# Kernel tuning notes

Measured on AMD Instinct MI355X. Metric: run time of the kernel, lower is better.

## Reference

```python
import jax, jax.numpy as jnp
import numpy as np

B, L, H, NH = 128, 512, 128, 2
HD = H // NH
NEG = -2.0**32 + 1  # matches torch paddings value


def _split_heads(x):
    # [B, L, H] -> [NH, B, L, HD]; equivalent to torch.cat(torch.split(x, HD, dim=2), dim=0)
    return x.reshape(B, L, NH, HD).transpose(2, 0, 1, 3)


def setup_inputs() -> dict:
    key = jax.random.key(0)
    ks = jax.random.split(key, 9)
    f = lambda k, s: jax.random.normal(k, s, dtype=jnp.float32)
    return {
        "queries": f(ks[0], (B, L, H)),
        "keys": f(ks[1], (B, L, H)),
        "neighbor_matrix": f(ks[2], (B, L, H)),
        "neighAt_matrix": f(ks[3], (B, L, H)),
        "abs_pos_K": f(ks[4], (B, L, H)),
        "abs_pos_V": f(ks[5], (B, L, H)),
        "Q_w": f(ks[6], (H, H)) * 0.05, "Q_b": jnp.zeros((H,), jnp.float32),
        "K_w": f(ks[7], (H, H)) * 0.05, "K_b": jnp.zeros((H,), jnp.float32),
        "V_w": f(ks[8], (H, H)) * 0.05, "V_b": jnp.zeros((H,), jnp.float32),
        # causal mask: True = masked, as used in NISRec (~tril)
        "attn_mask": ~jnp.tril(jnp.ones((L, L), dtype=bool)),
    }


def reference(queries, keys, neighbor_matrix, neighAt_matrix, abs_pos_K, abs_pos_V,
              Q_w, Q_b, K_w, K_b, V_w, V_b, attn_mask):
    Q = _split_heads(queries @ Q_w.T + Q_b)          # [NH,B,L,HD]
    K = _split_heads(keys @ K_w.T + K_b)
    V = _split_heads(keys @ V_w.T + V_b)
    nbr = _split_heads(neighbor_matrix)
    nat = _split_heads(neighAt_matrix)
    pk = _split_heads(abs_pos_K)
    pv = _split_heads(abs_pos_V)
    # sum of four Q.matmul(X^T) terms == Q.matmul((K+nbr+nat+pk)^T); same math, one GEMM
    logits = jnp.einsum('hbqd,hbkd->hbqk', Q, K + nbr + nat + pk)
    logits = logits / jnp.sqrt(jnp.asarray(HD, logits.dtype))
    logits = jnp.where(attn_mask[None, None, :, :], jnp.asarray(NEG, logits.dtype), logits)
    w = jax.nn.softmax(logits, axis=-1)  # dropout off (eval)
    # sum of four attn.matmul(X) terms == attn.matmul(V+nbr+nat+pv)
    out = jnp.einsum('hbqk,hbkd->hbqd', w, V + nbr + nat + pv)
    # merge heads back: torch.cat(torch.split(outputs, B, dim=0), dim=2)
    return out.transpose(1, 2, 0, 3).reshape(B, L, H)
```

## Files before the change

kernel.cpp:

```cpp
#include <hip/hip_runtime.h>

typedef __attribute__((ext_vector_type(8))) short bf16x8;
typedef __attribute__((ext_vector_type(4))) short bf16x4;
typedef __attribute__((ext_vector_type(4))) float f32x4;

#define NB 128
#define LL 512
#define HH 128
#define HDIM 64
#define NROWS (NB * LL)

__device__ __forceinline__ unsigned short f2b(float f) {
  unsigned int x = __float_as_uint(f);
  x = (x + 0x7fffu + ((x >> 16) & 1u)) >> 16;
  return (unsigned short)x;
}

__device__ __forceinline__ bf16x8 load8_cvt(const float* p) {
  float4 a = *(const float4*)p;
  float4 b = *(const float4*)(p + 4);
  bf16x8 r;
  r[0] = (short)f2b(a.x); r[1] = (short)f2b(a.y);
  r[2] = (short)f2b(a.z); r[3] = (short)f2b(a.w);
  r[4] = (short)f2b(b.x); r[5] = (short)f2b(b.y);
  r[6] = (short)f2b(b.z); r[7] = (short)f2b(b.w);
  return r;
}

#if __has_builtin(__builtin_amdgcn_mfma_f32_16x16x16bf16_1k)
__device__ __forceinline__ f32x4 mfma16(bf16x4 a, bf16x4 b, f32x4 c) {
  return __builtin_amdgcn_mfma_f32_16x16x16bf16_1k(a, b, c, 0, 0, 0);
}
#else
__device__ __forceinline__ f32x4 mfma16(bf16x4 a, bf16x4 b, f32x4 c) {
  asm volatile("s_nop 1\n\t"
               "v_mfma_f32_16x16x16_bf16 %0, %1, %2, %0\n\t"
               "s_nop 7\n\t"
               "s_nop 7"
               : "+v"(c) : "v"(a), "v"(b));
  return c;
}
#endif

__device__ __forceinline__ f32x4 mfma32(bf16x8 a, bf16x8 b, f32x4 c) {
  return __builtin_amdgcn_mfma_f32_16x16x32_bf16(a, b, c, 0, 0, 0);
}

__global__ __launch_bounds__(256) void wcvt_kernel(
    const float* __restrict__ Qw, const float* __restrict__ Kw,
    const float* __restrict__ Vw, unsigned short* __restrict__ Wb) {
  const int i = blockIdx.x * 256 + threadIdx.x;
  const float* src = (i < 4096) ? Qw : (i < 8192) ? Kw : Vw;
  const int off = (i & 4095) << 2;
  float4 v = *(const float4*)(src + off);
  ushort4 u;
  u.x = f2b(v.x); u.y = f2b(v.y); u.z = f2b(v.z); u.w = f2b(v.w);
  *(ushort4*)(Wb + ((size_t)i << 2)) = u;
}

__global__ __launch_bounds__(512) void fused_kernel(
    const float* __restrict__ queries, const float* __restrict__ keys,
    const float* __restrict__ nbr, const float* __restrict__ nat,
    const float* __restrict__ pk, const float* __restrict__ pv,
    const unsigned short* __restrict__ Wb, const float* __restrict__ Qbias,
    const float* __restrict__ Vbias, unsigned short* __restrict__ Vt,
    float* __restrict__ out) {
  __shared__ unsigned short wlds[2 * 128 * 128];
  __shared__ unsigned short klds[512 * 64];

  const int id = blockIdx.x;
  const int h = id >> 7;
  const int b = id & 127;
  const int tid = threadIdx.x;
  const int lane = tid & 63;
  const int w = tid >> 6;
  const int g = lane >> 4;
  const int qi = lane & 15;
  const int rswz = (qi & 7) << 4;

#pragma unroll
  for (int i = 0; i < 8; ++i) {
    const int byte = (tid + i * 512) * 16;
    const int row = (byte >> 8) & 127;
    *(bf16x8*)((char*)wlds + (byte ^ ((row & 7) << 4))) =
        *(const bf16x8*)((const char*)Wb + 32768 + byte);
  }
  __syncthreads();

  for (int rg = 0; rg < 4; ++rg) {
    const int l = w * 64 + rg * 16 + qi;
    const long roff = ((long)b * LL + l) * 128;

    bf16x8 xk[4];
#pragma unroll
    for (int kt = 0; kt < 4; ++kt)
      xk[kt] = load8_cvt(keys + roff + kt * 32 + g * 8);

    f32x4 accK[4];
#pragma unroll
    for (int ct = 0; ct < 4; ++ct) {
      accK[ct] = f32x4{0.f, 0.f, 0.f, 0.f};
      const int rw = h * 64 + ct * 16 + qi;
#pragma unroll
      for (int kt = 0; kt < 4; ++kt) {
        const int byte = rw * 256 + ((kt * 64 + g * 16) ^ rswz);
        bf16x8 wf = *(const bf16x8*)((const char*)wlds + byte);
        accK[ct] = mfma32(wf, xk[kt], accK[ct]);
      }
    }

    float4 tmp[4];
#pragma unroll
    for (int ct = 0; ct < 4; ++ct) {
      const int dl = ct * 16 + 4 * g;
      const int cg = h * 64 + dl;
      const float4 nb4 = *(const float4*)(nbr + roff + cg);
      const float4 na4 = *(const float4*)(nat + roff + cg);
      const float4 pk4 = *(const float4*)(pk + roff + cg);
      float4 t;
      t.x = nb4.x + na4.x; t.y = nb4.y + na4.y;
      t.z = nb4.z + na4.z; t.w = nb4.w + na4.w;
      tmp[ct] = t;
      ushort4 u;
      u.x = f2b(accK[ct][0] + t.x + pk4.x);
      u.y = f2b(accK[ct][1] + t.y + pk4.y);
      u.z = f2b(accK[ct][2] + t.z + pk4.z);
      u.w = f2b(accK[ct][3] + t.w + pk4.w);
      const int kb = l * 128 + dl * 2;
      *(ushort4*)((char*)klds + (kb ^ ((l & 7) << 4))) = u;
    }

    f32x4 accV[4];
#pragma unroll
    for (int ct = 0; ct < 4; ++ct) {
      accV[ct] = f32x4{0.f, 0.f, 0.f, 0.f};
      const int rw = h * 64 + ct * 16 + qi;
#pragma unroll
      for (int kt = 0; kt < 4; ++kt) {
        const int byte = 32768 + rw * 256 + ((kt * 64 + g * 16) ^ rswz);
        bf16x8 wf = *(const bf16x8*)((const char*)wlds + byte);
        accV[ct] = mfma32(wf, xk[kt], accV[ct]);
      }
    }
#pragma unroll
    for (int ct = 0; ct < 4; ++ct) {
      const int dl = ct * 16 + 4 * g;
      const int cg = h * 64 + dl;
      const float4 pv4 = *(const float4*)(pv + roff + cg);
      unsigned short* vp = Vt + (((long)h * NB + b) * HDIM + dl) * LL + l;
      vp[0 * LL] = f2b(accV[ct][0] + tmp[ct].x + pv4.x);
      vp[1 * LL] = f2b(accV[ct][1] + tmp[ct].y + pv4.y);
      vp[2 * LL] = f2b(accV[ct][2] + tmp[ct].z + pv4.z);
      vp[3 * LL] = f2b(accV[ct][3] + tmp[ct].w + pv4.w);
    }
  }

  __syncthreads();

#pragma unroll
  for (int i = 0; i < 4; ++i) {
    const int byte = (tid + i * 512) * 16;
    const int row = (byte >> 8) & 127;
    *(bf16x8*)((char*)wlds + (byte ^ ((row & 7) << 4))) =
        *(const bf16x8*)((const char*)Wb + byte);
  }
  __syncthreads();

  float vbe[4];
#pragma unroll
  for (int dt = 0; dt < 4; ++dt) vbe[dt] = Vbias[h * 64 + dt * 16 + qi];

  char* slot = (char*)wlds + 32768 + w * 2048;
  const unsigned short* Vbase = Vt + ((long)h * NB + b) * HDIM * LL;

  for (int half = 0; half < 2; ++half) {
    const int c = half ? w : 15 - w;
    const int qbase = c * 32;
    const int ntile = (c >> 1) + 1;

    bf16x8 qf[2][2];
#pragma unroll
    for (int q2 = 0; q2 < 2; ++q2) {
      const int l = qbase + q2 * 16 + qi;
      const long roff = ((long)b * LL + l) * 128;
      bf16x8 xq[4];
#pragma unroll
      for (int kt = 0; kt < 4; ++kt)
        xq[kt] = load8_cvt(queries + roff + kt * 32 + g * 8);
      f32x4 aq[4];
#pragma unroll
      for (int ct = 0; ct < 4; ++ct) {
        aq[ct] = f32x4{0.f, 0.f, 0.f, 0.f};
        const int rw = h * 64 + ct * 16 + qi;
#pragma unroll
        for (int kt = 0; kt < 4; ++kt) {
          const int byte = rw * 256 + ((kt * 64 + g * 16) ^ rswz);
          bf16x8 wf = *(const bf16x8*)((const char*)wlds + byte);
          aq[ct] = mfma32(wf, xq[kt], aq[ct]);
        }
      }
#pragma unroll
      for (int ct = 0; ct < 4; ++ct) {
        const int dl = ct * 16 + 4 * g;
        const float4 bv = *(const float4*)(Qbias + h * 64 + dl);
        ushort4 u;
        u.x = f2b(aq[ct][0] + bv.x);
        u.y = f2b(aq[ct][1] + bv.y);
        u.z = f2b(aq[ct][2] + bv.z);
        u.w = f2b(aq[ct][3] + bv.w);
        const int bb = qi * 128 + dl * 2;
        *(ushort4*)(slot + (bb ^ ((qi & 7) << 4))) = u;
      }
      asm volatile("s_waitcnt lgkmcnt(0)" ::: "memory");
      __builtin_amdgcn_sched_barrier(0);
      qf[q2][0] = *(const bf16x8*)(slot + ((qi * 128 + g * 16) ^ ((qi & 7) << 4)));
      qf[q2][1] = *(const bf16x8*)(slot + ((qi * 128 + 64 + g * 16) ^ ((qi & 7) << 4)));
    }

    f32x4 o[2][4];
#pragma unroll
    for (int q2 = 0; q2 < 2; ++q2)
#pragma unroll
      for (int dt = 0; dt < 4; ++dt) o[q2][dt] = f32x4{0.f, 0.f, 0.f, 0.f};
    float m[2] = {-1e30f, -1e30f};
    float lsum[2] = {0.f, 0.f};

    for (int it = 0; it < ntile; ++it) {
      const int k0 = it * 64;

      bf16x8 kf[4][2];
#pragma unroll
      for (int t = 0; t < 4; ++t) {
        const int l = k0 + t * 16 + qi;
        const int base = l * 128;
        const int sz = (l & 7) << 4;
        kf[t][0] = *(const bf16x8*)((char*)klds + ((base + g * 16) ^ sz));
        kf[t][1] = *(const bf16x8*)((char*)klds + ((base + 64 + g * 16) ^ sz));
      }

      bf16x4 vf[4][4];
#pragma unroll
      for (int dt = 0; dt < 4; ++dt)
#pragma unroll
        for (int t = 0; t < 4; ++t)
          vf[dt][t] = *(const bf16x4*)(Vbase + (dt * 16 + qi) * LL + k0 +
                                       t * 16 + 4 * g);

      f32x4 s[2][4];
#pragma unroll
      for (int q2 = 0; q2 < 2; ++q2)
#pragma unroll
        for (int t = 0; t < 4; ++t) {
          f32x4 acc = f32x4{0.f, 0.f, 0.f, 0.f};
          acc = mfma32(kf[t][0], qf[q2][0], acc);
          acc = mfma32(kf[t][1], qf[q2][1], acc);
          s[q2][t] = acc;
        }

      float alpha[2];
      bf16x4 pf[2][4];
#pragma unroll
      for (int q2 = 0; q2 < 2; ++q2) {
        const int myq = qbase + q2 * 16 + qi;
        float p[16];
        float pm = -1e30f;
#pragma unroll
        for (int t = 0; t < 4; ++t)
#pragma unroll
          for (int r = 0; r < 4; ++r) {
            float sv = s[q2][t][r] * 0.125f;
            const int key = k0 + t * 16 + 4 * g + r;
            sv = (key > myq) ? -1e30f : sv;
            p[t * 4 + r] = sv;
            pm = fmaxf(pm, sv);
          }
        pm = fmaxf(pm, __shfl_xor(pm, 16));
        pm = fmaxf(pm, __shfl_xor(pm, 32));
        const float mnew = fmaxf(m[q2], pm);
        alpha[q2] = exp2f((m[q2] - mnew) * 1.44269504f);
        float ps = 0.f;
#pragma unroll
        for (int i = 0; i < 16; ++i) {
          p[i] = exp2f((p[i] - mnew) * 1.44269504f);
          ps += p[i];
        }
        ps += __shfl_xor(ps, 16);
        ps += __shfl_xor(ps, 32);
        lsum[q2] = lsum[q2] * alpha[q2] + ps;
        m[q2] = mnew;
#pragma unroll
        for (int t = 0; t < 4; ++t) {
          pf[q2][t][0] = (short)f2b(p[t * 4 + 0]);
          pf[q2][t][1] = (short)f2b(p[t * 4 + 1]);
          pf[q2][t][2] = (short)f2b(p[t * 4 + 2]);
          pf[q2][t][3] = (short)f2b(p[t * 4 + 3]);
        }
      }

      float ar[2][4];
#pragma unroll
      for (int q2 = 0; q2 < 2; ++q2)
#pragma unroll
        for (int r = 0; r < 4; ++r) ar[q2][r] = __shfl(alpha[q2], 4 * g + r);

#pragma unroll
      for (int dt = 0; dt < 4; ++dt) {
#pragma unroll
        for (int q2 = 0; q2 < 2; ++q2) {
          o[q2][dt][0] *= ar[q2][0];
          o[q2][dt][1] *= ar[q2][1];
          o[q2][dt][2] *= ar[q2][2];
          o[q2][dt][3] *= ar[q2][3];
        }
#pragma unroll
        for (int t = 0; t < 4; ++t) {
          o[0][dt] = mfma16(pf[0][t], vf[dt][t], o[0][dt]);
          o[1][dt] = mfma16(pf[1][t], vf[dt][t], o[1][dt]);
        }
      }
    }

#pragma unroll
    for (int q2 = 0; q2 < 2; ++q2) {
      float linv[4];
#pragma unroll
      for (int r = 0; r < 4; ++r) linv[r] = 1.0f / __shfl(lsum[q2], 4 * g + r);
#pragma unroll
      for (int dt = 0; dt < 4; ++dt)
#pragma unroll
        for (int r = 0; r < 4; ++r) {
          const long row = (long)b * LL + qbase + q2 * 16 + 4 * g + r;
          out[row * HH + h * 64 + dt * 16 + qi] =
              o[q2][dt][r] * linv[r] + vbe[dt];
        }
    }
  }
}

extern "C" void kernel_launch(void* const* d_in, const int* in_sizes, int n_in,
                              void* d_out, int out_size, void* d_ws, size_t ws_size,
                              hipStream_t stream) {
  const float* queries = (const float*)d_in[0];
  const float* keys    = (const float*)d_in[1];
  const float* nbr     = (const float*)d_in[2];
  const float* nat     = (const float*)d_in[3];
  const float* pk      = (const float*)d_in[4];
  const float* pv      = (const float*)d_in[5];
  const float* Qw      = (const float*)d_in[6];
  const float* Qbias   = (const float*)d_in[7];
  const float* Kw      = (const float*)d_in[8];
  const float* Vw      = (const float*)d_in[10];
  const float* Vbias   = (const float*)d_in[11];

  unsigned short* Vt = (unsigned short*)d_ws;
  unsigned short* Wb = Vt + (size_t)2 * NB * HDIM * LL;

  wcvt_kernel<<<48, 256, 0, stream>>>(Qw, Kw, Vw, Wb);

  fused_kernel<<<256, 512, 0, stream>>>(queries, keys, nbr, nat, pk, pv, Wb,
                                        Qbias, Vbias, Vt, (float*)d_out);
}
```

Baseline: 85.76 us.

## Double block to 1024 threads with one 16-row query tile per wave

The fused kernel now runs 16 waves per block instead of 8. In the K/V projection phase each wave handles 32 rows instead of 64. In the attention phase each wave processes one 16-row query tile per half rather than two, with causal load balancing done by pairing tile j with 31-j. With only 256 blocks on the device, the goal is more resident waves per CU to hide memory and MFMA latency, and fewer live accumulators per thread. In exchange, K and V fragments are reused across fewer query rows, so each loaded fragment feeds half as many MFMAs. The 1024-thread launch bound also caps VGPRs per thread, which risks register spills.

```diff
diff --git a/kernel.cpp b/kernel.cpp
--- a/kernel.cpp
+++ b/kernel.cpp
@@ -58,7 +58,7 @@
   *(ushort4*)(Wb + ((size_t)i << 2)) = u;
 }
 
-__global__ __launch_bounds__(512) void fused_kernel(
+__global__ __launch_bounds__(1024) void fused_kernel(
     const float* __restrict__ queries, const float* __restrict__ keys,
     const float* __restrict__ nbr, const float* __restrict__ nat,
     const float* __restrict__ pk, const float* __restrict__ pv,
@@ -79,16 +79,17 @@
   const int rswz = (qi & 7) << 4;
 
 #pragma unroll
-  for (int i = 0; i < 8; ++i) {
-    const int byte = (tid + i * 512) * 16;
+  for (int i = 0; i < 4; ++i) {
+    const int byte = (tid + i * 1024) * 16;
     const int row = (byte >> 8) & 127;
     *(bf16x8*)((char*)wlds + (byte ^ ((row & 7) << 4))) =
         *(const bf16x8*)((const char*)Wb + 32768 + byte);
   }
   __syncthreads();
 
-  for (int rg = 0; rg < 4; ++rg) {
-    const int l = w * 64 + rg * 16 + qi;
+#pragma unroll
+  for (int rg = 0; rg < 2; ++rg) {
+    const int l = w * 32 + rg * 16 + qi;
     const long roff = ((long)b * LL + l) * 128;
 
     bf16x8 xk[4];
@@ -158,8 +159,8 @@
   __syncthreads();
 
 #pragma unroll
-  for (int i = 0; i < 4; ++i) {
-    const int byte = (tid + i * 512) * 16;
+  for (int i = 0; i < 2; ++i) {
+    const int byte = (tid + i * 1024) * 16;
     const int row = (byte >> 8) & 127;
     *(bf16x8*)((char*)wlds + (byte ^ ((row & 7) << 4))) =
         *(const bf16x8*)((const char*)Wb + byte);
@@ -174,56 +175,51 @@
   const unsigned short* Vbase = Vt + ((long)h * NB + b) * HDIM * LL;
 
   for (int half = 0; half < 2; ++half) {
-    const int c = half ? w : 15 - w;
-    const int qbase = c * 32;
-    const int ntile = (c >> 1) + 1;
-
-    bf16x8 qf[2][2];
-#pragma unroll
-    for (int q2 = 0; q2 < 2; ++q2) {
-      const int l = qbase + q2 * 16 + qi;
-      const long roff = ((long)b * LL + l) * 128;
-      bf16x8 xq[4];
-#pragma unroll
-      for (int kt = 0; kt < 4; ++kt)
-        xq[kt] = load8_cvt(queries + roff + kt * 32 + g * 8);
-      f32x4 aq[4];
-#pragma unroll
-      for (int ct = 0; ct < 4; ++ct) {
-        aq[ct] = f32x4{0.f, 0.f, 0.f, 0.f};
-        const int rw = h * 64 + ct * 16 + qi;
-#pragma unroll
-        for (int kt = 0; kt < 4; ++kt) {
-          const int byte = rw * 256 + ((kt * 64 + g * 16) ^ rswz);
-          bf16x8 wf = *(const bf16x8*)((const char*)wlds + byte);
-          aq[ct] = mfma32(wf, xq[kt], aq[ct]);
-        }
-      }
-#pragma unroll
-      for (int ct = 0; ct < 4; ++ct) {
-        const int dl = ct * 16 + 4 * g;
-        const float4 bv = *(const float4*)(Qbias + h * 64 + dl);
-        ushort4 u;
-        u.x = f2b(aq[ct][0] + bv.x);
-        u.y = f2b(aq[ct][1] + bv.y);
-        u.z = f2b(aq[ct][2] + bv.z);
-        u.w = f2b(aq[ct][3] + bv.w);
-        const int bb = qi * 128 + dl * 2;
-        *(ushort4*)(slot + (bb ^ ((qi & 7) << 4))) = u;
-      }
-      asm volatile("s_waitcnt lgkmcnt(0)" ::: "memory");
-      __builtin_amdgcn_sched_barrier(0);
-      qf[q2][0] = *(const bf16x8*)(slot + ((qi * 128 + g * 16) ^ ((qi & 7) << 4)));
-      qf[q2][1] = *(const bf16x8*)(slot + ((qi * 128 + 64 + g * 16) ^ ((qi & 7) << 4)));
-    }
-
-    f32x4 o[2][4];
-#pragma unroll
-    for (int q2 = 0; q2 < 2; ++q2)
-#pragma unroll
-      for (int dt = 0; dt < 4; ++dt) o[q2][dt] = f32x4{0.f, 0.f, 0.f, 0.f};
-    float m[2] = {-1e30f, -1e30f};
-    float lsum[2] = {0.f, 0.f};
+    const int j = half ? w : 31 - w;
+    const int qbase = j * 16;
+    const int myq = qbase + qi;
+    const int ntile = (j >> 2) + 1;
+
+    const long roff = ((long)b * LL + qbase + qi) * 128;
+    bf16x8 xq[4];
+#pragma unroll
+    for (int kt = 0; kt < 4; ++kt)
+      xq[kt] = load8_cvt(queries + roff + kt * 32 + g * 8);
+    f32x4 aq[4];
+#pragma unroll
+    for (int ct = 0; ct < 4; ++ct) {
+      aq[ct] = f32x4{0.f, 0.f, 0.f, 0.f};
+      const int rw = h * 64 + ct * 16 + qi;
+#pragma unroll
+      for (int kt = 0; kt < 4; ++kt) {
+        const int byte = rw * 256 + ((kt * 64 + g * 16) ^ rswz);
+        bf16x8 wf = *(const bf16x8*)((const char*)wlds + byte);
+        aq[ct] = mfma32(wf, xq[kt], aq[ct]);
+      }
+    }
+#pragma unroll
+    for (int ct = 0; ct < 4; ++ct) {
+      const int dl = ct * 16 + 4 * g;
+      const float4 bv = *(const float4*)(Qbias + h * 64 + dl);
+      ushort4 u;
+      u.x = f2b(aq[ct][0] + bv.x);
+      u.y = f2b(aq[ct][1] + bv.y);
+      u.z = f2b(aq[ct][2] + bv.z);
+      u.w = f2b(aq[ct][3] + bv.w);
+      const int bb = qi * 128 + dl * 2;
+      *(ushort4*)(slot + (bb ^ ((qi & 7) << 4))) = u;
+    }
+    asm volatile("s_waitcnt lgkmcnt(0)" ::: "memory");
+    __builtin_amdgcn_sched_barrier(0);
+    const bf16x8 qf0 =
+        *(const bf16x8*)(slot + ((qi * 128 + g * 16) ^ ((qi & 7) << 4)));
+    const bf16x8 qf1 =
+        *(const bf16x8*)(slot + ((qi * 128 + 64 + g * 16) ^ ((qi & 7) << 4)));
+
+    f32x4 o[4];
+#pragma unroll
+    for (int dt = 0; dt < 4; ++dt) o[dt] = f32x4{0.f, 0.f, 0.f, 0.f};
+    float m = -1e30f, lsum = 0.f;
 
     for (int it = 0; it < ntile; ++it) {
       const int k0 = it * 64;
@@ -246,94 +242,77 @@
           vf[dt][t] = *(const bf16x4*)(Vbase + (dt * 16 + qi) * LL + k0 +
                                        t * 16 + 4 * g);
 
-      f32x4 s[2][4];
-#pragma unroll
-      for (int q2 = 0; q2 < 2; ++q2)
-#pragma unroll
-        for (int t = 0; t < 4; ++t) {
-          f32x4 acc = f32x4{0.f, 0.f, 0.f, 0.f};
-          acc = mfma32(kf[t][0], qf[q2][0], acc);
-          acc = mfma32(kf[t][1], qf[q2][1], acc);
-          s[q2][t] = acc;
+      f32x4 s[4];
+#pragma unroll
+      for (int t = 0; t < 4; ++t) {
+        f32x4 acc = f32x4{0.f, 0.f, 0.f, 0.f};
+        acc = mfma32(kf[t][0], qf0, acc);
+        acc = mfma32(kf[t][1], qf1, acc);
+        s[t] = acc;
+      }
+
+      float p[16];
+      float pm = -1e30f;
+#pragma unroll
+      for (int t = 0; t < 4; ++t)
+#pragma unroll
+        for (int r = 0; r < 4; ++r) {
+          float sv = s[t][r] * 0.125f;
+          const int key = k0 + t * 16 + 4 * g + r;
+          sv = (key > myq) ? -1e30f : sv;
+          p[t * 4 + r] = sv;
+          pm = fmaxf(pm, sv);
         }
-
-      float alpha[2];
-      bf16x4 pf[2][4];
-#pragma unroll
-      for (int q2 = 0; q2 < 2; ++q2) {
-        const int myq = qbase + q2 * 16 + qi;
-        float p[16];
-        float pm = -1e30f;
+      pm = fmaxf(pm, __shfl_xor(pm, 16));
+      pm = fmaxf(pm, __shfl_xor(pm, 32));
+      const float mnew = fmaxf(m, pm);
+      const float alpha = exp2f((m - mnew) * 1.44269504f);
+      float ps = 0.f;
+#pragma unroll
+      for (int i = 0; i < 16; ++i) {
+        p[i] = exp2f((p[i] - mnew) * 1.44269504f);
+        ps += p[i];
+      }
+      ps += __shfl_xor(ps, 16);
+      ps += __shfl_xor(ps, 32);
+      lsum = lsum * alpha + ps;
+      m = mnew;
+
+      bf16x4 pf[4];
+#pragma unroll
+      for (int t = 0; t < 4; ++t) {
+        pf[t][0] = (short)f2b(p[t * 4 + 0]);
+        pf[t][1] = (short)f2b(p[t * 4 + 1]);
+        pf[t][2] = (short)f2b(p[t * 4 + 2]);
+        pf[t][3] = (short)f2b(p[t * 4 + 3]);
+      }
+
+      float ar[4];
+#pragma unroll
+      for (int r = 0; r < 4; ++r) ar[r] = __shfl(alpha, 4 * g + r);
+
+#pragma unroll
+      for (int dt = 0; dt < 4; ++dt) {
+        o[dt][0] *= ar[0];
+        o[dt][1] *= ar[1];
+        o[dt][2] *= ar[2];
+        o[dt][3] *= ar[3];
 #pragma unroll
         for (int t = 0; t < 4; ++t)
-#pragma unroll
-          for (int r = 0; r < 4; ++r) {
-            float sv = s[q2][t][r] * 0.125f;
-            const int key = k0 + t * 16 + 4 * g + r;
-            sv = (key > myq) ? -1e30f : sv;
-            p[t * 4 + r] = sv;
-            pm = fmaxf(pm, sv);
-          }
-        pm = fmaxf(pm, __shfl_xor(pm, 16));
-        pm = fmaxf(pm, __shfl_xor(pm, 32));
-        const float mnew = fmaxf(m[q2], pm);
-        alpha[q2] = exp2f((m[q2] - mnew) * 1.44269504f);
-        float ps = 0.f;
-#pragma unroll
-        for (int i = 0; i < 16; ++i) {
-          p[i] = exp2f((p[i] - mnew) * 1.44269504f);
-          ps += p[i];
-        }
-        ps += __shfl_xor(ps, 16);
-        ps += __shfl_xor(ps, 32);
-        lsum[q2] = lsum[q2] * alpha[q2] + ps;
-        m[q2] = mnew;
-#pragma unroll
-        for (int t = 0; t < 4; ++t) {
-          pf[q2][t][0] = (short)f2b(p[t * 4 + 0]);
-          pf[q2][t][1] = (short)f2b(p[t * 4 + 1]);
-          pf[q2][t][2] = (short)f2b(p[t * 4 + 2]);
-          pf[q2][t][3] = (short)f2b(p[t * 4 + 3]);
-        }
-      }
-
-      float ar[2][4];
-#pragma unroll
-      for (int q2 = 0; q2 < 2; ++q2)
-#pragma unroll
-        for (int r = 0; r < 4; ++r) ar[q2][r] = __shfl(alpha[q2], 4 * g + r);
-
-#pragma unroll
-      for (int dt = 0; dt < 4; ++dt) {
-#pragma unroll
-        for (int q2 = 0; q2 < 2; ++q2) {
-          o[q2][dt][0] *= ar[q2][0];
-          o[q2][dt][1] *= ar[q2][1];
-          o[q2][dt][2] *= ar[q2][2];
-          o[q2][dt][3] *= ar[q2][3];
-        }
-#pragma unroll
-        for (int t = 0; t < 4; ++t) {
-          o[0][dt] = mfma16(pf[0][t], vf[dt][t], o[0][dt]);
-          o[1][dt] = mfma16(pf[1][t], vf[dt][t], o[1][dt]);
-        }
-      }
-    }
-
-#pragma unroll
-    for (int q2 = 0; q2 < 2; ++q2) {
-      float linv[4];
-#pragma unroll
-      for (int r = 0; r < 4; ++r) linv[r] = 1.0f / __shfl(lsum[q2], 4 * g + r);
-#pragma unroll
-      for (int dt = 0; dt < 4; ++dt)
-#pragma unroll
-        for (int r = 0; r < 4; ++r) {
-          const long row = (long)b * LL + qbase + q2 * 16 + 4 * g + r;
-          out[row * HH + h * 64 + dt * 16 + qi] =
-              o[q2][dt][r] * linv[r] + vbe[dt];
-        }
-    }
+          o[dt] = mfma16(pf[t], vf[dt][t], o[dt]);
+      }
+    }
+
+    float linv[4];
+#pragma unroll
+    for (int r = 0; r < 4; ++r) linv[r] = 1.0f / __shfl(lsum, 4 * g + r);
+#pragma unroll
+    for (int dt = 0; dt < 4; ++dt)
+#pragma unroll
+      for (int r = 0; r < 4; ++r) {
+        const long row = (long)b * LL + qbase + 4 * g + r;
+        out[row * HH + h * 64 + dt * 16 + qi] = o[dt][r] * linv[r] + vbe[dt];
+      }
   }
 }
 
@@ -357,6 +336,6 @@
 
   wcvt_kernel<<<48, 256, 0, stream>>>(Qw, Kw, Vw, Wb);
 
-  fused_kernel<<<256, 512, 0, stream>>>(queries, keys, nbr, nat, pk, pv, Wb,
-                                        Qbias, Vbias, Vt, (float*)d_out);
-}
+  fused_kernel<<<256, 1024, 0, stream>>>(queries, keys, nbr, nat, pk, pv, Wb,
+                                         Qbias, Vbias, Vt, (float*)d_out);
+}
```

Result: slower. 132.3 us (+54.3%).

## Software-pipeline key and stream global loads across row groups with manual waitcnt

Applied to the files above, without the earlier changes.

Replaces the compiler-scheduled loads in the K/V projection loop with inline-asm global_load_dwordx4 calls. The next row group's keys are prefetched, and the nbr/nat/pk/pv loads are issued before the K MFMAs, with explicit s_waitcnt vmcnt counts and scheduling barriers. The aim is to overlap global memory latency with MFMA work. It also adds a min-blocks-per-CU hint of 2 to launch_bounds, which caps registers. Hand-counted vmcnt values depend on exact load and store ordering, and the tighter register budget could cause spills.

```diff
diff --git a/kernel.cpp b/kernel.cpp
--- a/kernel.cpp
+++ b/kernel.cpp
@@ -27,6 +27,15 @@
   return r;
 }
 
+__device__ __forceinline__ bf16x8 cvt2(float4 a, float4 b) {
+  bf16x8 r;
+  r[0] = (short)f2b(a.x); r[1] = (short)f2b(a.y);
+  r[2] = (short)f2b(a.z); r[3] = (short)f2b(a.w);
+  r[4] = (short)f2b(b.x); r[5] = (short)f2b(b.y);
+  r[6] = (short)f2b(b.z); r[7] = (short)f2b(b.w);
+  return r;
+}
+
 #if __has_builtin(__builtin_amdgcn_mfma_f32_16x16x16bf16_1k)
 __device__ __forceinline__ f32x4 mfma16(bf16x4 a, bf16x4 b, f32x4 c) {
   return __builtin_amdgcn_mfma_f32_16x16x16bf16_1k(a, b, c, 0, 0, 0);
@@ -45,6 +54,14 @@
 __device__ __forceinline__ f32x4 mfma32(bf16x8 a, bf16x8 b, f32x4 c) {
   return __builtin_amdgcn_mfma_f32_16x16x32_bf16(a, b, c, 0, 0, 0);
 }
+
+#define GLOAD(dst, base, OFF)                                        \
+  asm volatile("global_load_dwordx4 %0, %1, off offset:" #OFF        \
+               : "=v"(dst) : "v"(base))
+
+#define VWAIT(N)                                                     \
+  asm volatile("s_waitcnt vmcnt(" #N ")" ::: "memory");              \
+  __builtin_amdgcn_sched_barrier(0)
 
 __global__ __launch_bounds__(256) void wcvt_kernel(
     const float* __restrict__ Qw, const float* __restrict__ Kw,
@@ -58,7 +75,7 @@
   *(ushort4*)(Wb + ((size_t)i << 2)) = u;
 }
 
-__global__ __launch_bounds__(512) void fused_kernel(
+__global__ __launch_bounds__(512, 2) void fused_kernel(
     const float* __restrict__ queries, const float* __restrict__ keys,
     const float* __restrict__ nbr, const float* __restrict__ nat,
     const float* __restrict__ pk, const float* __restrict__ pv,
@@ -85,75 +102,116 @@
     *(bf16x8*)((char*)wlds + (byte ^ ((row & 7) << 4))) =
         *(const bf16x8*)((const char*)Wb + 32768 + byte);
   }
+
+  float4 ky0, ky1, ky2, ky3, ky4, ky5, ky6, ky7;
+  float4 nb0, nb1, nb2, nb3, na0, na1, na2, na3;
+  float4 pk0, pk1, pk2, pk3, pv0, pv1, pv2, pv3;
+  bf16x8 xk0, xk1, xk2, xk3;
+
+#define ISSUE_KEYS(RG)                                                       \
+  {                                                                          \
+    const float* kb =                                                        \
+        keys + ((long)b * LL + w * 64 + (RG) * 16 + qi) * 128 + g * 8;       \
+    GLOAD(ky0, kb, 0);   GLOAD(ky1, kb, 16);                                 \
+    GLOAD(ky2, kb, 128); GLOAD(ky3, kb, 144);                                \
+    GLOAD(ky4, kb, 256); GLOAD(ky5, kb, 272);                                \
+    GLOAD(ky6, kb, 384); GLOAD(ky7, kb, 400);                                \
+  }
+
+#define ISSUE_STREAMS(RG)                                                    \
+  {                                                                          \
+    const long ro =                                                          \
+        ((long)b * LL + w * 64 + (RG) * 16 + qi) * 128 + h * 64 + 4 * g;     \
+    const float* p1 = nbr + ro; const float* p2 = nat + ro;                  \
+    const float* p3 = pk + ro;  const float* p4 = pv + ro;                   \
+    GLOAD(nb0, p1, 0); GLOAD(nb1, p1, 64); GLOAD(nb2, p1, 128); GLOAD(nb3, p1, 192); \
+    GLOAD(na0, p2, 0); GLOAD(na1, p2, 64); GLOAD(na2, p2, 128); GLOAD(na3, p2, 192); \
+    GLOAD(pk0, p3, 0); GLOAD(pk1, p3, 64); GLOAD(pk2, p3, 128); GLOAD(pk3, p3, 192); \
+    GLOAD(pv0, p4, 0); GLOAD(pv1, p4, 64); GLOAD(pv2, p4, 128); GLOAD(pv3, p4, 192); \
+  }
+
+#define KEPI_CT(l, CT, NBv, NAv, PKv, TMPv)                                  \
+  {                                                                          \
+    TMPv.x = NBv.x + NAv.x; TMPv.y = NBv.y + NAv.y;                          \
+    TMPv.z = NBv.z + NAv.z; TMPv.w = NBv.w + NAv.w;                          \
+    ushort4 u;                                                               \
+    u.x = f2b(accK[CT][0] + TMPv.x + PKv.x);                                 \
+    u.y = f2b(accK[CT][1] + TMPv.y + PKv.y);                                 \
+    u.z = f2b(accK[CT][2] + TMPv.z + PKv.z);                                 \
+    u.w = f2b(accK[CT][3] + TMPv.w + PKv.w);                                 \
+    const int kb2 = (l) * 128 + ((CT) * 16 + 4 * g) * 2;                     \
+    *(ushort4*)((char*)klds + (kb2 ^ (((l) & 7) << 4))) = u;                 \
+  }
+
+#define VEPI_CT(l, CT, PVv, TMPv)                                            \
+  {                                                                          \
+    const int dl = (CT) * 16 + 4 * g;                                        \
+    unsigned short* vp = Vt + (((long)h * NB + b) * HDIM + dl) * LL + (l);   \
+    vp[0 * LL] = f2b(accV[CT][0] + TMPv.x + PVv.x);                          \
+    vp[1 * LL] = f2b(accV[CT][1] + TMPv.y + PVv.y);                          \
+    vp[2 * LL] = f2b(accV[CT][2] + TMPv.z + PVv.z);                          \
+    vp[3 * LL] = f2b(accV[CT][3] + TMPv.w + PVv.w);                          \
+  }
+
+#define RG_STEP(RG, W0, W1, LAST)                                            \
+  {                                                                          \
+    const int l = w * 64 + (RG) * 16 + qi;                                   \
+    VWAIT(W0);                                                               \
+    xk0 = cvt2(ky0, ky1); xk1 = cvt2(ky2, ky3);                              \
+    xk2 = cvt2(ky4, ky5); xk3 = cvt2(ky6, ky7);                              \
+    ISSUE_STREAMS(RG);                                                       \
+    if (!(LAST)) ISSUE_KEYS((RG) + 1);                                       \
+    f32x4 accK[4];                                                           \
+    _Pragma("unroll") for (int ct = 0; ct < 4; ++ct) {                       \
+      accK[ct] = f32x4{0.f, 0.f, 0.f, 0.f};                                  \
+      const int rw = h * 64 + ct * 16 + qi;                                  \
+      {                                                                      \
+        bf16x8 wf;                                                           \
+        wf = *(const bf16x8*)((const char*)wlds + rw * 256 + ((0 * 64 + g * 16) ^ rswz)); \
+        accK[ct] = mfma32(wf, xk0, accK[ct]);                                \
+        wf = *(const bf16x8*)((const char*)wlds + rw * 256 + ((1 * 64 + g * 16) ^ rswz)); \
+        accK[ct] = mfma32(wf, xk1, accK[ct]);                                \
+        wf = *(const bf16x8*)((const char*)wlds + rw * 256 + ((2 * 64 + g * 16) ^ rswz)); \
+        accK[ct] = mfma32(wf, xk2, accK[ct]);                                \
+        wf = *(const bf16x8*)((const char*)wlds + rw * 256 + ((3 * 64 + g * 16) ^ rswz)); \
+        accK[ct] = mfma32(wf, xk3, accK[ct]);                                \
+      }                                                                      \
+    }                                                                        \
+    VWAIT(W1);                                                               \
+    float4 tmp0, tmp1, tmp2, tmp3;                                           \
+    KEPI_CT(l, 0, nb0, na0, pk0, tmp0);                                      \
+    KEPI_CT(l, 1, nb1, na1, pk1, tmp1);                                      \
+    KEPI_CT(l, 2, nb2, na2, pk2, tmp2);                                      \
+    KEPI_CT(l, 3, nb3, na3, pk3, tmp3);                                      \
+    f32x4 accV[4];                                                           \
+    _Pragma("unroll") for (int ct = 0; ct < 4; ++ct) {                       \
+      accV[ct] = f32x4{0.f, 0.f, 0.f, 0.f};                                  \
+      const int rw = h * 64 + ct * 16 + qi;                                  \
+      {                                                                      \
+        bf16x8 wf;                                                           \
+        wf = *(const bf16x8*)((const char*)wlds + 32768 + rw * 256 + ((0 * 64 + g * 16) ^ rswz)); \
+        accV[ct] = mfma32(wf, xk0, accV[ct]);                                \
+        wf = *(const bf16x8*)((const char*)wlds + 32768 + rw * 256 + ((1 * 64 + g * 16) ^ rswz)); \
+        accV[ct] = mfma32(wf, xk1, accV[ct]);                                \
+        wf = *(const bf16x8*)((const char*)wlds + 32768 + rw * 256 + ((2 * 64 + g * 16) ^ rswz)); \
+        accV[ct] = mfma32(wf, xk2, accV[ct]);                                \
+        wf = *(const bf16x8*)((const char*)wlds + 32768 + rw * 256 + ((3 * 64 + g * 16) ^ rswz)); \
+        accV[ct] = mfma32(wf, xk3, accV[ct]);                                \
+      }                                                                      \
+    }                                                                        \
+    VEPI_CT(l, 0, pv0, tmp0);                                                \
+    VEPI_CT(l, 1, pv1, tmp1);                                                \
+    VEPI_CT(l, 2, pv2, tmp2);                                                \
+    VEPI_CT(l, 3, pv3, tmp3);                                                \
+  }
+
+  ISSUE_KEYS(0);
   __syncthreads();
 
-  for (int rg = 0; rg < 4; ++rg) {
-    const int l = w * 64 + rg * 16 + qi;
-    const long roff = ((long)b * LL + l) * 128;
-
-    bf16x8 xk[4];
-#pragma unroll
-    for (int kt = 0; kt < 4; ++kt)
-      xk[kt] = load8_cvt(keys + roff + kt * 32 + g * 8);
-
-    f32x4 accK[4];
-#pragma unroll
-    for (int ct = 0; ct < 4; ++ct) {
-      accK[ct] = f32x4{0.f, 0.f, 0.f, 0.f};
-      const int rw = h * 64 + ct * 16 + qi;
-#pragma unroll
-      for (int kt = 0; kt < 4; ++kt) {
-        const int byte = rw * 256 + ((kt * 64 + g * 16) ^ rswz);
-        bf16x8 wf = *(const bf16x8*)((const char*)wlds + byte);
-        accK[ct] = mfma32(wf, xk[kt], accK[ct]);
-      }
-    }
-
-    float4 tmp[4];
-#pragma unroll
-    for (int ct = 0; ct < 4; ++ct) {
-      const int dl = ct * 16 + 4 * g;
-      const int cg = h * 64 + dl;
-      const float4 nb4 = *(const float4*)(nbr + roff + cg);
-      const float4 na4 = *(const float4*)(nat + roff + cg);
-      const float4 pk4 = *(const float4*)(pk + roff + cg);
-      float4 t;
-      t.x = nb4.x + na4.x; t.y = nb4.y + na4.y;
-      t.z = nb4.z + na4.z; t.w = nb4.w + na4.w;
-      tmp[ct] = t;
-      ushort4 u;
-      u.x = f2b(accK[ct][0] + t.x + pk4.x);
-      u.y = f2b(accK[ct][1] + t.y + pk4.y);
-      u.z = f2b(accK[ct][2] + t.z + pk4.z);
-      u.w = f2b(accK[ct][3] + t.w + pk4.w);
-      const int kb = l * 128 + dl * 2;
-      *(ushort4*)((char*)klds + (kb ^ ((l & 7) << 4))) = u;
-    }
-
-    f32x4 accV[4];
-#pragma unroll
-    for (int ct = 0; ct < 4; ++ct) {
-      accV[ct] = f32x4{0.f, 0.f, 0.f, 0.f};
-      const int rw = h * 64 + ct * 16 + qi;
-#pragma unroll
-      for (int kt = 0; kt < 4; ++kt) {
-        const int byte = 32768 + rw * 256 + ((kt * 64 + g * 16) ^ rswz);
-        bf16x8 wf = *(const bf16x8*)((const char*)wlds + byte);
-        accV[ct] = mfma32(wf, xk[kt], accV[ct]);
-      }
-    }
-#pragma unroll
-    for (int ct = 0; ct < 4; ++ct) {
-      const int dl = ct * 16 + 4 * g;
-      const int cg = h * 64 + dl;
-      const float4 pv4 = *(const float4*)(pv + roff + cg);
-      unsigned short* vp = Vt + (((long)h * NB + b) * HDIM + dl) * LL + l;
-      vp[0 * LL] = f2b(accV[ct][0] + tmp[ct].x + pv4.x);
-      vp[1 * LL] = f2b(accV[ct][1] + tmp[ct].y + pv4.y);
-      vp[2 * LL] = f2b(accV[ct][2] + tmp[ct].z + pv4.z);
-      vp[3 * LL] = f2b(accV[ct][3] + tmp[ct].w + pv4.w);
-    }
-  }
+  RG_STEP(0, 0, 8, 0);
+  RG_STEP(1, 16, 8, 0);
+  RG_STEP(2, 16, 8, 0);
+  RG_STEP(3, 16, 0, 1);
 
   __syncthreads();
 
```

Result: no change. 84.63 us (median of 2 runs) (-1.3%).

## Move K buffer from LDS to global workspace and load only per-head weights

Applied to the files above, without the earlier changes.

The combined K tensor now goes to a global workspace buffer instead of a 64KB LDS array, and the attention loop reads it back from global memory (likely L2-resident). Only the current head's K, V and Q weight slices are staged, all at once, into a single 64KB LDS buffer, which removes the second weight reload and its barrier. The launch bounds now request higher occupancy. The cost is extra global write and read traffic for K. With only 256 blocks the occupancy hint may not matter, and K loads from global have higher latency than LDS.

```diff
diff --git a/kernel.cpp b/kernel.cpp
--- a/kernel.cpp
+++ b/kernel.cpp
@@ -58,15 +58,14 @@
   *(ushort4*)(Wb + ((size_t)i << 2)) = u;
 }
 
-__global__ __launch_bounds__(512) void fused_kernel(
+__global__ __launch_bounds__(512, 4) void fused_kernel(
     const float* __restrict__ queries, const float* __restrict__ keys,
     const float* __restrict__ nbr, const float* __restrict__ nat,
     const float* __restrict__ pk, const float* __restrict__ pv,
     const unsigned short* __restrict__ Wb, const float* __restrict__ Qbias,
     const float* __restrict__ Vbias, unsigned short* __restrict__ Vt,
-    float* __restrict__ out) {
-  __shared__ unsigned short wlds[2 * 128 * 128];
-  __shared__ unsigned short klds[512 * 64];
+    unsigned short* __restrict__ Kt, float* __restrict__ out) {
+  __shared__ unsigned short wlds[32768];
 
   const int id = blockIdx.x;
   const int h = id >> 7;
@@ -78,12 +77,19 @@
   const int qi = lane & 15;
   const int rswz = (qi & 7) << 4;
 
-#pragma unroll
-  for (int i = 0; i < 8; ++i) {
-    const int byte = (tid + i * 512) * 16;
-    const int row = (byte >> 8) & 127;
-    *(bf16x8*)((char*)wlds + (byte ^ ((row & 7) << 4))) =
-        *(const bf16x8*)((const char*)Wb + 32768 + byte);
+  unsigned short* Ktb = Kt + ((long)h * NB + b) * LL * HDIM;
+
+  {
+    const int srcb[3] = {32768 + h * 16384, 65536 + h * 16384, h * 16384};
+#pragma unroll
+    for (int i = 0; i < 6; ++i) {
+      const int idx = tid + i * 512;
+      const int s = idx >> 10;
+      const int byte = (idx & 1023) * 16;
+      const int r = byte >> 8;
+      *(bf16x8*)((char*)wlds + s * 16384 + (byte ^ ((r & 7) << 4))) =
+          *(const bf16x8*)((const char*)Wb + srcb[s] + byte);
+    }
   }
   __syncthreads();
 
@@ -100,11 +106,11 @@
 #pragma unroll
     for (int ct = 0; ct < 4; ++ct) {
       accK[ct] = f32x4{0.f, 0.f, 0.f, 0.f};
-      const int rw = h * 64 + ct * 16 + qi;
+      const int rwb = (ct * 16 + qi) * 256;
 #pragma unroll
       for (int kt = 0; kt < 4; ++kt) {
-        const int byte = rw * 256 + ((kt * 64 + g * 16) ^ rswz);
-        bf16x8 wf = *(const bf16x8*)((const char*)wlds + byte);
+        bf16x8 wf = *(const bf16x8*)((const char*)wlds + rwb +
+                                     ((kt * 64 + g * 16) ^ rswz));
         accK[ct] = mfma32(wf, xk[kt], accK[ct]);
       }
     }
@@ -126,19 +132,18 @@
       u.y = f2b(accK[ct][1] + t.y + pk4.y);
       u.z = f2b(accK[ct][2] + t.z + pk4.z);
       u.w = f2b(accK[ct][3] + t.w + pk4.w);
-      const int kb = l * 128 + dl * 2;
-      *(ushort4*)((char*)klds + (kb ^ ((l & 7) << 4))) = u;
+      *(ushort4*)(Ktb + (long)l * HDIM + dl) = u;
     }
 
     f32x4 accV[4];
 #pragma unroll
     for (int ct = 0; ct < 4; ++ct) {
       accV[ct] = f32x4{0.f, 0.f, 0.f, 0.f};
-      const int rw = h * 64 + ct * 16 + qi;
+      const int rwb = 16384 + (ct * 16 + qi) * 256;
 #pragma unroll
       for (int kt = 0; kt < 4; ++kt) {
-        const int byte = 32768 + rw * 256 + ((kt * 64 + g * 16) ^ rswz);
-        bf16x8 wf = *(const bf16x8*)((const char*)wlds + byte);
+        bf16x8 wf = *(const bf16x8*)((const char*)wlds + rwb +
+                                     ((kt * 64 + g * 16) ^ rswz));
         accV[ct] = mfma32(wf, xk[kt], accV[ct]);
       }
     }
@@ -157,20 +162,11 @@
 
   __syncthreads();
 
-#pragma unroll
-  for (int i = 0; i < 4; ++i) {
-    const int byte = (tid + i * 512) * 16;
-    const int row = (byte >> 8) & 127;
-    *(bf16x8*)((char*)wlds + (byte ^ ((row & 7) << 4))) =
-        *(const bf16x8*)((const char*)Wb + byte);
-  }
-  __syncthreads();
-
   float vbe[4];
 #pragma unroll
   for (int dt = 0; dt < 4; ++dt) vbe[dt] = Vbias[h * 64 + dt * 16 + qi];
 
-  char* slot = (char*)wlds + 32768 + w * 2048;
+  char* slot = (char*)wlds + 49152 + w * 2048;
   const unsigned short* Vbase = Vt + ((long)h * NB + b) * HDIM * LL;
 
   for (int half = 0; half < 2; ++half) {
@@ -191,11 +187,11 @@
 #pragma unroll
       for (int ct = 0; ct < 4; ++ct) {
         aq[ct] = f32x4{0.f, 0.f, 0.f, 0.f};
-        const int rw = h * 64 + ct * 16 + qi;
+        const int rwb = 32768 + (ct * 16 + qi) * 256;
 #pragma unroll
         for (int kt = 0; kt < 4; ++kt) {
-          const int byte = rw * 256 + ((kt * 64 + g * 16) ^ rswz);
-          bf16x8 wf = *(const bf16x8*)((const char*)wlds + byte);
+          bf16x8 wf = *(const bf16x8*)((const char*)wlds + rwb +
+                                       ((kt * 64 + g * 16) ^ rswz));
           aq[ct] = mfma32(wf, xq[kt], aq[ct]);
         }
       }
@@ -231,11 +227,9 @@
       bf16x8 kf[4][2];
 #pragma unroll
       for (int t = 0; t < 4; ++t) {
-        const int l = k0 + t * 16 + qi;
-        const int base = l * 128;
-        const int sz = (l & 7) << 4;
-        kf[t][0] = *(const bf16x8*)((char*)klds + ((base + g * 16) ^ sz));
-        kf[t][1] = *(const bf16x8*)((char*)klds + ((base + 64 + g * 16) ^ sz));
+        const unsigned short* kr = Ktb + (long)(k0 + t * 16 + qi) * HDIM;
+        kf[t][0] = *(const bf16x8*)(kr + g * 8);
+        kf[t][1] = *(const bf16x8*)(kr + 32 + g * 8);
       }
 
       bf16x4 vf[4][4];
@@ -353,10 +347,11 @@
   const float* Vbias   = (const float*)d_in[11];
 
   unsigned short* Vt = (unsigned short*)d_ws;
-  unsigned short* Wb = Vt + (size_t)2 * NB * HDIM * LL;
+  unsigned short* Kt = Vt + (size_t)2 * NB * HDIM * LL;
+  unsigned short* Wb = Kt + (size_t)2 * NB * LL * HDIM;
 
   wcvt_kernel<<<48, 256, 0, stream>>>(Qw, Kw, Vw, Wb);
 
   fused_kernel<<<256, 512, 0, stream>>>(queries, keys, nbr, nat, pk, pv, Wb,
-                                        Qbias, Vbias, Vt, (float*)d_out);
-}
+                                        Qbias, Vbias, Vt, Kt, (float*)d_out);
+}
```

Result: slower. 182.2 us (+112.5%).
